# Optimization experiments

Hardware: AMD Instinct MI355X
Metric: run time of the kernel (lower is better)

## Reference

```python
import jax, jax.numpy as jnp
import numpy as np

B, L, H, K = 16, 2048, 1024, 4  # batch, seq, hidden, heads
NEG = -1e9  # stand-in for -inf in masked softmax (grad-safe, prob ~0)

def setup_inputs() -> dict:
    key = jax.random.key(0)
    ks = jax.random.split(key, 6)
    s = 0.02
    hidden = jax.random.normal(ks[0], (B, L, H), dtype=jnp.float32)
    masks = jax.random.randint(ks[1], (B, L), 0, 2).astype(jnp.bool_)
    Wp = jax.random.normal(ks[2], (H, H * K), dtype=jnp.float32) * s
    W1 = jax.random.normal(ks[3], (K, H, H // 2), dtype=jnp.float32) * s
    b1 = jax.random.normal(ks[4], (K, H // 2), dtype=jnp.float32) * s
    W2 = jax.random.normal(ks[5], (K, H // 2), dtype=jnp.float32) * s
    return {"hidden": hidden, "masks": masks, "Wp": Wp, "W1": W1, "b1": b1, "W2": W2}

def reference(hidden, masks, Wp, W1, b1, W2):
    b, l, h = hidden.shape
    k = W1.shape[0]
    # projection (no bias), split into heads: [b,l,k,h]
    proj = (hidden @ Wp).reshape(b, l, k, h)
    # per-head tanh MLP score: Linear(h, h//2)+bias -> tanh -> Linear(h//2, 1)
    a1 = jnp.tanh(jnp.einsum('blkh,khd->blkd', proj, W1) + b1)  # [b,l,k,h//2]
    logits = jnp.einsum('blkd,kd->kbl', a1, W2)                 # [k,b,l]
    # masked softmax over sequence dim
    logits = jnp.where(masks[None, :, :], NEG, logits)
    attn = jax.nn.softmax(logits, axis=-1)                      # [k,b,l]
    return attn
```

## Files before the change

kernel.cpp:

```cpp
#include <hip/hip_runtime.h>
#include <hip/hip_bf16.h>
#include <cstdint>
#include <cstddef>

#define HD   1024
#define NK   4
#define DD   512
#define LSEQ 2048
#define NB   16
#define MTOT (NB*LSEQ)
#define NF2  (NK*DD)

typedef __attribute__((ext_vector_type(4))) float f32x4;
typedef __attribute__((ext_vector_type(8))) short bf16x8;

#define GLOAD16(gp, lp) __builtin_amdgcn_global_load_lds( \
    (const __attribute__((address_space(1))) void*)(gp),  \
    (__attribute__((address_space(3))) void*)(lp), 16, 0, 0)

static __device__ __forceinline__ ushort f2bf(float f) {
  union { float f; unsigned u; } x; x.f = f;
  unsigned r = x.u + 0x7FFFu + ((x.u >> 16) & 1u);
  return (ushort)(r >> 16);
}

static __device__ __forceinline__ float fast_tanh(float x) {
  x = fminf(fmaxf(x, -15.f), 15.f);
  float t = __expf(2.0f * x);
  return (t - 1.0f) / (t + 1.0f);
}

__global__ void detect_mask_kernel(const unsigned char* __restrict__ m, int nbytes,
                                   int* __restrict__ flag) {
  int found = 0;
  for (int i = blockIdx.x * blockDim.x + threadIdx.x; i < nbytes;
       i += gridDim.x * blockDim.x)
    if ((i & 3) && m[i]) found = 1;
  if (__any(found) && (threadIdx.x & 63) == 0) atomicOr(flag, 1);
}

__global__ void cvt_f32_bf16_kernel(const float* __restrict__ src,
                                    ushort* __restrict__ dst, long n) {
  long stride = (long)gridDim.x * blockDim.x * 4;
  for (long i = ((long)blockIdx.x * blockDim.x + threadIdx.x) * 4; i < n; i += stride) {
    f32x4 v = *(const f32x4*)(src + i);
    ushort4 o; o.x = f2bf(v.x); o.y = f2bf(v.y); o.z = f2bf(v.z); o.w = f2bf(v.w);
    *(ushort4*)(dst + i) = o;
  }
}

__global__ void cvt_wp_heads_kernel(const float* __restrict__ Wp,
                                    ushort* __restrict__ WpH) {
  long i4 = ((long)blockIdx.x * blockDim.x + threadIdx.x) * 4;
  int h = (int)(i4 >> 20);
  int c = (int)((i4 >> 10) & 1023);
  int j = (int)(i4 & 1023);
  f32x4 v = *(const f32x4*)(Wp + (long)c * (NK * HD) + h * HD + j);
  ushort4 o; o.x = f2bf(v.x); o.y = f2bf(v.y); o.z = f2bf(v.z); o.w = f2bf(v.w);
  *(ushort4*)(WpH + i4) = o;
}

__global__ void transpose_cvt_kernel(const float* __restrict__ src,
                                     ushort* __restrict__ dst,
                                     int R, int C, long sBatch, long dBatch) {
  __shared__ float tile[32][33];
  const float* s = src + blockIdx.z * sBatch;
  ushort* d = dst + blockIdx.z * dBatch;
  int c0 = blockIdx.x * 32, r0 = blockIdx.y * 32;
  int tx = threadIdx.x, ty = threadIdx.y;
  #pragma unroll
  for (int i = 0; i < 32; i += 8)
    tile[ty + i][tx] = s[(long)(r0 + ty + i) * C + (c0 + tx)];
  __syncthreads();
  #pragma unroll
  for (int i = 0; i < 32; i += 8)
    d[(long)(c0 + ty + i) * R + (r0 + tx)] = f2bf(tile[tx][ty + i]);
}

template<int MODE>
__global__ __launch_bounds__(512, 2)
void gemm256_kernel(const ushort* __restrict__ A, int lda, long aZs,
                    const ushort* __restrict__ Bt, int ldb, long bZs, int Kdim,
                    ushort* __restrict__ Cout, int ldc, long cZs,
                    const float* __restrict__ b1, const float* __restrict__ W2,
                    float* __restrict__ partialOut, int m0glob) {
  __shared__ __align__(16) char lds[131072];

  const int tid = threadIdx.x;
  const int w = tid >> 6, lane = tid & 63;
  const int z = blockIdx.z;

  const int bid = blockIdx.x + gridDim.x * blockIdx.y;
  const int nMB = gridDim.x, nNB = gridDim.y;
  int m0, n0;
  if ((nMB & 7) == 0) {
    const int x = bid & 7, j = bid >> 3;
    const int mi = x * (nMB >> 3) + j / nNB;
    const int ni = j % nNB;
    m0 = mi * 256; n0 = ni * 256;
  } else {
    m0 = (bid % nMB) * 256; n0 = (bid / nMB) * 256;
  }

  const ushort* Ag = A + z * aZs + (long)m0 * lda;
  const ushort* Bg = Bt + z * bZs + (long)n0 * ldb;

  const int wm = w >> 2, wn = w & 3;
  const int rsel = lane & 15;
  const int chunkC = ((lane >> 4) ^ ((rsel >> 1) & 3)) << 4;
  const int laneA = wm * 8192 + rsel * 64 + chunkC;
  const int laneB = 65536 + wn * 4096 + rsel * 64 + chunkC;

  const int stCg = ((lane & 3) ^ ((lane >> 3) & 3)) * 8;
  const int stR0 = (w * 2) * 16 + (lane >> 2);
  const int stDst0 = (w * 2) * 1024;

  #define STAGE(gbase, ld, regionByte, dsl, ktile, kh)                          \
    {                                                                           \
      _Pragma("unroll")                                                         \
      for (int jj = 0; jj < 2; ++jj) {                                          \
        const ushort* gp = (gbase) + (long)(stR0 + jj * 16) * (ld) +            \
                           ((ktile) << 6) + ((kh) << 5) + stCg;                 \
        GLOAD16(gp, lds + (regionByte) + (dsl) * 16384 + stDst0 + jj * 1024);   \
      }                                                                         \
    }

  f32x4 acc[8][4] = {};

  STAGE(Ag, lda, 0,     0, 0, 0);
  STAGE(Bg, ldb, 65536, 0, 0, 0);
  STAGE(Ag, lda, 0,     1, 0, 1);
  STAGE(Bg, ldb, 65536, 1, 0, 1);
  asm volatile("s_waitcnt vmcnt(4)" ::: "memory");
  __builtin_amdgcn_sched_barrier(0);
  __builtin_amdgcn_s_barrier();

  const int nt = Kdim >> 6;
  for (int t = 0; t < nt; ++t) {
    const int ts = (t + 1 < nt) ? t + 1 : t;
    const int s0 = (2 * t) & 3, s1 = (2 * t + 1) & 3;
    const int p0 = (2 * t + 2) & 3, p1 = (2 * t + 3) & 3;
    bf16x8 aF[4], bB[4];
    #pragma unroll
    for (int q = 0; q < 4; ++q) {
      const int kk = q >> 1, mh = q & 1;
      const int slot = (kk ? s1 : s0) * 16384;
      if (mh == 0) {
        #pragma unroll
        for (int nf = 0; nf < 4; ++nf)
          bB[nf] = *(const bf16x8*)(lds + slot + laneB + nf * 1024);
      }
      #pragma unroll
      for (int mf = 0; mf < 4; ++mf)
        aF[mf] = *(const bf16x8*)(lds + slot + laneA + mh * 4096 + mf * 1024);
      if (q == 0)      STAGE(Ag, lda, 0,     p0, ts, 0)
      else if (q == 1) STAGE(Bg, ldb, 65536, p0, ts, 0)
      else if (q == 2) STAGE(Ag, lda, 0,     p1, ts, 1)
      else             STAGE(Bg, ldb, 65536, p1, ts, 1)
      __builtin_amdgcn_s_barrier();
      __builtin_amdgcn_s_setprio(1);
      #pragma unroll
      for (int mf = 0; mf < 4; ++mf)
        #pragma unroll
        for (int nf = 0; nf < 4; ++nf)
          acc[mh * 4 + mf][nf] = __builtin_amdgcn_mfma_f32_16x16x32_bf16(
              aF[mf], bB[nf], acc[mh * 4 + mf][nf], 0, 0, 0);
      __builtin_amdgcn_s_setprio(0);
      if (q & 1) {
        asm volatile("s_waitcnt vmcnt(4)" ::: "memory");
        __builtin_amdgcn_sched_barrier(0);
      }
      __builtin_amdgcn_s_barrier();
    }
  }
  asm volatile("s_waitcnt vmcnt(0)" ::: "memory");

  if constexpr (MODE == 0) {
    #pragma unroll
    for (int mf = 0; mf < 8; ++mf)
      #pragma unroll
      for (int nf = 0; nf < 4; ++nf) {
        const int col = n0 + wn * 64 + nf * 16 + (lane & 15);
        #pragma unroll
        for (int r = 0; r < 4; ++r) {
          const int row = m0 + wm * 128 + mf * 16 + ((lane >> 4) << 2) + r;
          Cout[z * cZs + (long)row * ldc + col] = f2bf(acc[mf][nf][r]);
        }
      }
  } else {
    float b1v[4], w2v[4];
    #pragma unroll
    for (int nf = 0; nf < 4; ++nf) {
      const int col = n0 + wn * 64 + nf * 16 + (lane & 15);
      b1v[nf] = b1[col];
      w2v[nf] = W2[col];
    }
    const int wslice = (n0 + wn * 64) >> 6;
    float* pb = partialOut + (long)wslice * MTOT + m0glob + m0 + wm * 128;
    #pragma unroll
    for (int mf = 0; mf < 8; ++mf)
      #pragma unroll
      for (int r = 0; r < 4; ++r) {
        float s = 0.f;
        #pragma unroll
        for (int nf = 0; nf < 4; ++nf)
          s += fast_tanh(acc[mf][nf][r] + b1v[nf]) * w2v[nf];
        s += __shfl_xor(s, 1, 64);
        s += __shfl_xor(s, 2, 64);
        s += __shfl_xor(s, 4, 64);
        s += __shfl_xor(s, 8, 64);
        if ((lane & 15) == 0)
          pb[mf * 16 + ((lane >> 4) << 2) + r] = s;
      }
  }
  #undef STAGE
}

__global__ __launch_bounds__(256)
void masked_softmax_kernel(const float* __restrict__ partial,
                           const unsigned char* __restrict__ maskB,
                           const int* __restrict__ maskI,
                           const int* __restrict__ flag,
                           float* __restrict__ out) {
  const int kb = blockIdx.x;
  const int k = kb >> 4, b = kb & (NB - 1);
  const long base = (long)kb * LSEQ;
  const bool isByte = (*flag != 0);
  const int tid = threadIdx.x;
  const float* pk = partial + (long)(k * 8) * MTOT + (long)b * LSEQ;

  float x[8];
  float mx = -3.0e38f;
  #pragma unroll
  for (int j = 0; j < 8; ++j) {
    int l = tid + j * 256;
    float v = 0.f;
    #pragma unroll
    for (int ws = 0; ws < 8; ++ws) v += pk[(long)ws * MTOT + l];
    bool msk = isByte ? (maskB[b * LSEQ + l] != 0) : (maskI[b * LSEQ + l] != 0);
    v = msk ? -1e9f : v;
    x[j] = v; mx = fmaxf(mx, v);
  }
  __shared__ float redm[4], reds[4];
  #pragma unroll
  for (int off = 32; off >= 1; off >>= 1) mx = fmaxf(mx, __shfl_xor(mx, off, 64));
  if ((tid & 63) == 0) redm[tid >> 6] = mx;
  __syncthreads();
  mx = fmaxf(fmaxf(redm[0], redm[1]), fmaxf(redm[2], redm[3]));

  float sum = 0.f;
  #pragma unroll
  for (int j = 0; j < 8; ++j) { x[j] = __expf(x[j] - mx); sum += x[j]; }
  #pragma unroll
  for (int off = 32; off >= 1; off >>= 1) sum += __shfl_xor(sum, off, 64);
  if ((tid & 63) == 0) reds[tid >> 6] = sum;
  __syncthreads();
  sum = reds[0] + reds[1] + reds[2] + reds[3];

  float inv = 1.0f / sum;
  #pragma unroll
  for (int j = 0; j < 8; ++j) out[base + tid + j * 256] = x[j] * inv;
}

extern "C" void kernel_launch(void* const* d_in, const int* in_sizes, int n_in,
                              void* d_out, int out_size, void* d_ws, size_t ws_size,
                              hipStream_t stream) {
  const float* hidden = (const float*)d_in[0];
  const void*  masks  = d_in[1];
  const float* Wp     = (const float*)d_in[2];
  const float* W1     = (const float*)d_in[3];
  const float* b1     = (const float*)d_in[4];
  const float* W2     = (const float*)d_in[5];
  float* out = (float*)d_out;

  char* ws = (char*)d_ws;
  ushort* W1T      = (ushort*)(ws + 0);
  ushort* WpH      = (ushort*)(ws + 4194304);
  ushort* WfT      = (ushort*)(ws + 12582912);
  float*  partial  = (float*) (ws + 16777216);
  int*    flag     = (int*)   (ws + 20971520);
  ushort* hiddenBf = (ushort*)(ws + 20971776);

  const size_t fixedBytes = 20971776;
  size_t avail = (ws_size > fixedBytes) ? (ws_size - fixedBytes) : 0;
  long chunkM = (long)(avail / ((long)HD * 2)) & ~255L;
  if (chunkM > MTOT) chunkM = MTOT;
  if (chunkM < 256) chunkM = 256;

  hipMemsetAsync(flag, 0, 256, stream);

  detect_mask_kernel<<<8, 256, 0, stream>>>((const unsigned char*)masks, NB * LSEQ, flag);

  dim3 tb(32, 8);
  transpose_cvt_kernel<<<dim3(DD / 32, HD / 32, NK), tb, 0, stream>>>(
      W1, W1T, HD, DD, (long)HD * DD, (long)DD * HD);
  cvt_wp_heads_kernel<<<4096, 256, 0, stream>>>(Wp, WpH);

  gemm256_kernel<0><<<dim3(2, 4, 4), 512, 0, stream>>>(
      W1T, HD, (long)DD * HD,
      WpH, HD, (long)HD * HD, HD,
      WfT, HD, (long)DD * HD,
      nullptr, nullptr, nullptr, 0);

  for (long m0 = 0; m0 < MTOT; m0 += chunkM) {
    long cm = chunkM; if (m0 + cm > MTOT) cm = MTOT - m0;
    cvt_f32_bf16_kernel<<<2048, 256, 0, stream>>>(
        hidden + m0 * HD, hiddenBf, cm * HD);
    gemm256_kernel<1><<<dim3(cm / 256, NF2 / 256, 1), 512, 0, stream>>>(
        hiddenBf, HD, 0,
        WfT, HD, 0, HD,
        nullptr, 0, 0,
        b1, W2, partial, (int)m0);
  }

  masked_softmax_kernel<<<NK * NB, 256, 0, stream>>>(
      partial, (const unsigned char*)masks, (const int*)masks, flag, out);
}
```

Baseline: 252.7 us.

## Replace pipelined 256x256 GEMM with simple single-buffered 128x128 tile GEMM

Swaps the 512-thread 256x256 tiled GEMM, which used a 4-slot LDS ring with asynchronous prefetch and priority scheduling, for a 256-thread 128x128 tile kernel. The new kernel loads one 32-wide K slice into 16KB of LDS and synchronizes twice per step, with no overlap between loads and MFMA. The aim is presumably more blocks and higher occupancy from the smaller LDS footprint. In exchange it gives up the software pipelining and halves per-block data reuse, so more global traffic and more exposed load latency are likely.

```diff
diff --git a/kernel.cpp b/kernel.cpp
--- a/kernel.cpp
+++ b/kernel.cpp
@@ -78,16 +78,16 @@
 }
 
 template<int MODE>
-__global__ __launch_bounds__(512, 2)
-void gemm256_kernel(const ushort* __restrict__ A, int lda, long aZs,
+__global__ __launch_bounds__(256, 2)
+void gemm128_kernel(const ushort* __restrict__ A, int lda, long aZs,
                     const ushort* __restrict__ Bt, int ldb, long bZs, int Kdim,
                     ushort* __restrict__ Cout, int ldc, long cZs,
                     const float* __restrict__ b1, const float* __restrict__ W2,
                     float* __restrict__ partialOut, int m0glob) {
-  __shared__ __align__(16) char lds[131072];
+  __shared__ __align__(16) char lds[16384];
 
   const int tid = threadIdx.x;
-  const int w = tid >> 6, lane = tid & 63;
+  const int wave = tid >> 6, lane = tid & 63;
   const int z = blockIdx.z;
 
   const int bid = blockIdx.x + gridDim.x * blockIdx.y;
@@ -95,95 +95,61 @@
   int m0, n0;
   if ((nMB & 7) == 0) {
     const int x = bid & 7, j = bid >> 3;
-    const int mi = x * (nMB >> 3) + j / nNB;
-    const int ni = j % nNB;
-    m0 = mi * 256; n0 = ni * 256;
+    m0 = (x * (nMB >> 3) + j / nNB) * 128;
+    n0 = (j % nNB) * 128;
   } else {
-    m0 = (bid % nMB) * 256; n0 = (bid / nMB) * 256;
+    m0 = (bid % nMB) * 128; n0 = (bid / nMB) * 128;
   }
 
   const ushort* Ag = A + z * aZs + (long)m0 * lda;
   const ushort* Bg = Bt + z * bZs + (long)n0 * ldb;
 
-  const int wm = w >> 2, wn = w & 3;
-  const int rsel = lane & 15;
-  const int chunkC = ((lane >> 4) ^ ((rsel >> 1) & 3)) << 4;
-  const int laneA = wm * 8192 + rsel * 64 + chunkC;
-  const int laneB = 65536 + wn * 4096 + rsel * 64 + chunkC;
-
+  const int wr = wave >> 1, wc = wave & 1;
+  const int rsel = lane & 15, ch = lane >> 4;
+  const int chunkC = (ch ^ ((rsel >> 1) & 3)) << 4;
+  const int laneA = wr * 4096 + rsel * 64 + chunkC;
+  const int laneB = 8192 + wc * 4096 + rsel * 64 + chunkC;
+
+  const int stRow = wave * 16 + (lane >> 2);
   const int stCg = ((lane & 3) ^ ((lane >> 3) & 3)) * 8;
-  const int stR0 = (w * 2) * 16 + (lane >> 2);
-  const int stDst0 = (w * 2) * 1024;
-
-  #define STAGE(gbase, ld, regionByte, dsl, ktile, kh)                          \
-    {                                                                           \
-      _Pragma("unroll")                                                         \
-      for (int jj = 0; jj < 2; ++jj) {                                          \
-        const ushort* gp = (gbase) + (long)(stR0 + jj * 16) * (ld) +            \
-                           ((ktile) << 6) + ((kh) << 5) + stCg;                 \
-        GLOAD16(gp, lds + (regionByte) + (dsl) * 16384 + stDst0 + jj * 1024);   \
-      }                                                                         \
-    }
-
-  f32x4 acc[8][4] = {};
-
-  STAGE(Ag, lda, 0,     0, 0, 0);
-  STAGE(Bg, ldb, 65536, 0, 0, 0);
-  STAGE(Ag, lda, 0,     1, 0, 1);
-  STAGE(Bg, ldb, 65536, 1, 0, 1);
-  asm volatile("s_waitcnt vmcnt(4)" ::: "memory");
-  __builtin_amdgcn_sched_barrier(0);
-  __builtin_amdgcn_s_barrier();
-
-  const int nt = Kdim >> 6;
-  for (int t = 0; t < nt; ++t) {
-    const int ts = (t + 1 < nt) ? t + 1 : t;
-    const int s0 = (2 * t) & 3, s1 = (2 * t + 1) & 3;
-    const int p0 = (2 * t + 2) & 3, p1 = (2 * t + 3) & 3;
-    bf16x8 aF[4], bB[4];
-    #pragma unroll
-    for (int q = 0; q < 4; ++q) {
-      const int kk = q >> 1, mh = q & 1;
-      const int slot = (kk ? s1 : s0) * 16384;
-      if (mh == 0) {
-        #pragma unroll
-        for (int nf = 0; nf < 4; ++nf)
-          bB[nf] = *(const bf16x8*)(lds + slot + laneB + nf * 1024);
-      }
+  const int ldsOff = wave * 1024;
+
+  f32x4 acc[4][4] = {};
+
+  const int ksteps = Kdim >> 5;
+  for (int kt = 0; kt < ksteps; ++kt) {
+    const int kk = (kt << 5) + stCg;
+    GLOAD16(Ag + (long)(m0 ? 0 : 0, stRow) * lda + kk,        (char*)lds + ldsOff);
+    GLOAD16(Ag + (long)(64 + stRow) * lda + kk,               (char*)lds + 4096 + ldsOff);
+    GLOAD16(Bg + (long)(stRow) * ldb + kk,                    (char*)lds + 8192 + ldsOff);
+    GLOAD16(Bg + (long)(64 + stRow) * ldb + kk,               (char*)lds + 12288 + ldsOff);
+    __syncthreads();
+
+    bf16x8 aF[4], bF[4];
+    #pragma unroll
+    for (int mf = 0; mf < 4; ++mf)
+      aF[mf] = *(const bf16x8*)(lds + laneA + mf * 1024);
+    #pragma unroll
+    for (int nf = 0; nf < 4; ++nf)
+      bF[nf] = *(const bf16x8*)(lds + laneB + nf * 1024);
+    #pragma unroll
+    for (int mf = 0; mf < 4; ++mf)
       #pragma unroll
-      for (int mf = 0; mf < 4; ++mf)
-        aF[mf] = *(const bf16x8*)(lds + slot + laneA + mh * 4096 + mf * 1024);
-      if (q == 0)      STAGE(Ag, lda, 0,     p0, ts, 0)
-      else if (q == 1) STAGE(Bg, ldb, 65536, p0, ts, 0)
-      else if (q == 2) STAGE(Ag, lda, 0,     p1, ts, 1)
-      else             STAGE(Bg, ldb, 65536, p1, ts, 1)
-      __builtin_amdgcn_s_barrier();
-      __builtin_amdgcn_s_setprio(1);
-      #pragma unroll
-      for (int mf = 0; mf < 4; ++mf)
-        #pragma unroll
-        for (int nf = 0; nf < 4; ++nf)
-          acc[mh * 4 + mf][nf] = __builtin_amdgcn_mfma_f32_16x16x32_bf16(
-              aF[mf], bB[nf], acc[mh * 4 + mf][nf], 0, 0, 0);
-      __builtin_amdgcn_s_setprio(0);
-      if (q & 1) {
-        asm volatile("s_waitcnt vmcnt(4)" ::: "memory");
-        __builtin_amdgcn_sched_barrier(0);
-      }
-      __builtin_amdgcn_s_barrier();
-    }
-  }
-  asm volatile("s_waitcnt vmcnt(0)" ::: "memory");
+      for (int nf = 0; nf < 4; ++nf)
+        acc[mf][nf] = __builtin_amdgcn_mfma_f32_16x16x32_bf16(
+            aF[mf], bF[nf], acc[mf][nf], 0, 0, 0);
+    __syncthreads();
+  }
 
   if constexpr (MODE == 0) {
     #pragma unroll
-    for (int mf = 0; mf < 8; ++mf)
+    for (int mf = 0; mf < 4; ++mf)
       #pragma unroll
       for (int nf = 0; nf < 4; ++nf) {
-        const int col = n0 + wn * 64 + nf * 16 + (lane & 15);
+        const int col = n0 + wc * 64 + nf * 16 + (lane & 15);
         #pragma unroll
         for (int r = 0; r < 4; ++r) {
-          const int row = m0 + wm * 128 + mf * 16 + ((lane >> 4) << 2) + r;
+          const int row = m0 + wr * 64 + mf * 16 + ((lane >> 4) << 2) + r;
           Cout[z * cZs + (long)row * ldc + col] = f2bf(acc[mf][nf][r]);
         }
       }
@@ -191,14 +157,14 @@
     float b1v[4], w2v[4];
     #pragma unroll
     for (int nf = 0; nf < 4; ++nf) {
-      const int col = n0 + wn * 64 + nf * 16 + (lane & 15);
+      const int col = n0 + wc * 64 + nf * 16 + (lane & 15);
       b1v[nf] = b1[col];
       w2v[nf] = W2[col];
     }
-    const int wslice = (n0 + wn * 64) >> 6;
-    float* pb = partialOut + (long)wslice * MTOT + m0glob + m0 + wm * 128;
-    #pragma unroll
-    for (int mf = 0; mf < 8; ++mf)
+    const int wslice = (n0 + wc * 64) >> 6;
+    float* pb = partialOut + (long)wslice * MTOT + m0glob + m0 + wr * 64;
+    #pragma unroll
+    for (int mf = 0; mf < 4; ++mf)
       #pragma unroll
       for (int r = 0; r < 4; ++r) {
         float s = 0.f;
@@ -213,7 +179,6 @@
           pb[mf * 16 + ((lane >> 4) << 2) + r] = s;
       }
   }
-  #undef STAGE
 }
 
 __global__ __launch_bounds__(256)
@@ -283,9 +248,9 @@
 
   const size_t fixedBytes = 20971776;
   size_t avail = (ws_size > fixedBytes) ? (ws_size - fixedBytes) : 0;
-  long chunkM = (long)(avail / ((long)HD * 2)) & ~255L;
+  long chunkM = (long)(avail / ((long)HD * 2)) & ~127L;
   if (chunkM > MTOT) chunkM = MTOT;
-  if (chunkM < 256) chunkM = 256;
+  if (chunkM < 128) chunkM = 128;
 
   hipMemsetAsync(flag, 0, 256, stream);
 
@@ -296,7 +261,7 @@
       W1, W1T, HD, DD, (long)HD * DD, (long)DD * HD);
   cvt_wp_heads_kernel<<<4096, 256, 0, stream>>>(Wp, WpH);
 
-  gemm256_kernel<0><<<dim3(2, 4, 4), 512, 0, stream>>>(
+  gemm128_kernel<0><<<dim3(DD / 128, HD / 128, NK), 256, 0, stream>>>(
       W1T, HD, (long)DD * HD,
       WpH, HD, (long)HD * HD, HD,
       WfT, HD, (long)DD * HD,
@@ -306,7 +271,7 @@
     long cm = chunkM; if (m0 + cm > MTOT) cm = MTOT - m0;
     cvt_f32_bf16_kernel<<<2048, 256, 0, stream>>>(
         hidden + m0 * HD, hiddenBf, cm * HD);
-    gemm256_kernel<1><<<dim3(cm / 256, NF2 / 256, 1), 512, 0, stream>>>(
+    gemm128_kernel<1><<<dim3(cm / 128, NF2 / 128, 1), 256, 0, stream>>>(
         hiddenBf, HD, 0,
         WfT, HD, 0, HD,
         nullptr, 0, 0,
```

Measured after the change: 255.6 us. About the same (+1.1%).
